# Optimization experiments

Hardware: AMD Instinct MI355X
Metric: run time of the kernel (lower is better)

Reference implementation:

```python
import jax, jax.numpy as jnp
import numpy as np

HEADS = 8
HEAD_DIM = 160
L_TXT = 77
C = 3  # number of erased target concepts
SIG_A, SIG_B, SIG_C = 10.0, 0.5, 1.0
EPS = 1e-8


def setup_inputs() -> dict:
    key = jax.random.key(0)
    ks = jax.random.split(key, 8)
    B, S, D, DX = 8, 1024, 1280, 768
    return {
        "hidden_states": jax.random.normal(ks[0], (B, S, D), jnp.float32),
        "encoder_hidden_states": jax.random.normal(ks[1], (B, L_TXT, DX), jnp.float32),
        "Wq": jax.random.normal(ks[2], (D, D), jnp.float32) * 0.02,
        "Wk": jax.random.normal(ks[3], (DX, D), jnp.float32) * 0.02,
        "Wv": jax.random.normal(ks[4], (DX, D), jnp.float32) * 0.02,
        "Wo": jax.random.normal(ks[5], (D, D), jnp.float32) * 0.02,
        "bo": jnp.zeros((D,), jnp.float32),
        "target_value": jax.random.normal(ks[7], (2 * C * HEADS, L_TXT, HEAD_DIM), jnp.float32),
    }


def _head_to_batch(x):
    B, S, D = x.shape
    return x.reshape(B, S, HEADS, D // HEADS).transpose(0, 2, 1, 3).reshape(B * HEADS, S, D // HEADS)


def _ortho_decomp_retain(v, target_value):
    # v: [M, 77, d]  (M = batch*heads, with batch = 2*R from CFG)
    d = HEAD_DIM
    hd = 16 * d
    # regroup target records: [2*C*8,77,d] -> [C,16,77,d]
    tar = target_value.reshape(2, C, HEADS, L_TXT, d).transpose(1, 0, 2, 3, 4).reshape(C, 16, L_TXT, d)
    T = tar.transpose(2, 0, 1, 3).reshape(L_TXT, C, hd)  # [77, C, 16d] per-token concept vectors
    # one-step Gram-Schmidt projection matrix per token (uses ORIGINAL V_j, as in source)
    G = jnp.einsum('lcd,led->lce', T, T)                  # [77, C, C] Gram matrix
    diag = jnp.einsum('lcc->lc', G)                       # [77, C]
    Pm = jnp.eye(C, dtype=v.dtype) - jnp.tril(G / diag[:, None, :], -1)  # [77, C, C]
    OB = jnp.einsum('lce,led->lcd', Pm, T)                # ortho basis [77, C, 16d]
    # regroup current value into records of 16 (=2*8) maps
    M = v.shape[0]
    R = M // 16
    cur = v.reshape(2, R, HEADS, L_TXT, d).transpose(1, 0, 2, 3, 4).reshape(R, 16, L_TXT, d)
    pro = cur.transpose(0, 2, 1, 3).reshape(R, L_TXT, hd)  # [R, 77, 16d]
    dot1 = jnp.einsum('lcd,rld->rlc', OB, pro)             # [R, 77, C]
    dot2 = jnp.sum(OB * OB, axis=-1)                       # [77, C]
    w = jnp.nan_to_num(dot1 / dot2)
    w = w.at[:, 0, :].set(0.0)                             # weight[0].fill_(0): zero token 0 (BOS)
    # token_sim: cosine similarity + sigmoid gating
    nT = jnp.maximum(jnp.linalg.norm(T, axis=-1), EPS)     # [77, C]
    nP = jnp.maximum(jnp.linalg.norm(pro, axis=-1), EPS)   # [R, 77]
    cos = jnp.einsum('lcd,rld->rlc', T, pro) / (nT[None] * nP[:, :, None])
    cos = SIG_C / (1.0 + jnp.exp(-SIG_A * (cos - SIG_B)))
    PB = jnp.einsum('lce,rled->rlcd', Pm, cos[..., None] * T)  # projected basis [R,77,C,16d]
    era = jnp.einsum('rlc,rlcd->rld', w, PB)               # [R, 77, 16d]
    era = era.reshape(R, L_TXT, 16, d).transpose(0, 2, 1, 3)  # [R, 16, 77, d]
    ret = cur - era                                        # retain branch
    return ret.reshape(R, 2, HEADS, L_TXT, d).transpose(1, 0, 2, 3, 4).reshape(M, L_TXT, d)


def reference(hidden_states, encoder_hidden_states, Wq, Wk, Wv, Wo, bo, target_value):
    B, S, D = hidden_states.shape
    q = _head_to_batch(hidden_states @ Wq)            # [B*h, S, d]
    k = _head_to_batch(encoder_hidden_states @ Wk)    # [B*h, 77, d]
    v = _head_to_batch(encoder_hidden_states @ Wv)    # [B*h, 77, d]
    scale = 1.0 / jnp.sqrt(jnp.asarray(HEAD_DIM, q.dtype))
    probs = jax.nn.softmax(jnp.einsum('bqd,bkd->bqk', q, k) * scale, axis=-1)
    v = _ortho_decomp_retain(v, target_value)         # concept-erased (retain) values
    hs = jnp.einsum('bqk,bkd->bqd', probs, v)         # [B*h, S, d]
    hs = hs.reshape(B, HEADS, S, HEAD_DIM).transpose(0, 2, 1, 3).reshape(B, S, D)
    return hs @ Wo + bo
```

## Files before the change

### kernel.cpp

```cpp
#include <hip/hip_runtime.h>
#include <hip/hip_bf16.h>
#include <math.h>

#define BATCH   8
#define S_LEN   1024
#define D_MODEL 1280
#define DX      768
#define NH      8
#define HD      160
#define LTXT    77
#define NBH     (BATCH*NH)
#define MKV_PAD 640
#define MQ      (BATCH*S_LEN)
#define MKV     (BATCH*LTXT)

typedef _Float16 f16x8 __attribute__((ext_vector_type(8)));
typedef _Float16 f16x4 __attribute__((ext_vector_type(4)));
typedef float    f32x4 __attribute__((ext_vector_type(4)));

#define NB_HID 10240
#define NB_ENC 480
#define NB_WQ  1600
#define NB_WO  1600
#define NB_WK  960
#define NB_WV  960
#define NB_PREP (NB_HID+NB_ENC+NB_WQ+NB_WO+NB_WK+NB_WV)

__device__ inline void to_f16_dev(const float* __restrict__ X,
                                  _Float16* __restrict__ Y,
                                  int K, int Mreal, int bid)
{
    const size_t g = ((size_t)bid * 256 + threadIdx.x) * 4;
    const int row = (int)(g / K);
    float4 x = make_float4(0.f, 0.f, 0.f, 0.f);
    if (row < Mreal) x = *(const float4*)&X[g];
    f16x4 o;
    o[0] = (_Float16)x.x; o[1] = (_Float16)x.y;
    o[2] = (_Float16)x.z; o[3] = (_Float16)x.w;
    *(f16x4*)&Y[g] = o;
}

__device__ inline void wt_t_dev(const float* __restrict__ W,
                                _Float16* __restrict__ BT,
                                int K, int N, int KLD, int noff,
                                int bx, int by, float (*tile)[33])
{
    const int k0 = by * 32, n0 = bx * 32;
    const int tx = threadIdx.x & 31, ty = threadIdx.x >> 5;
#pragma unroll
    for (int r = 0; r < 32; r += 8)
        tile[r + ty][tx] = W[(size_t)(k0 + r + ty) * N + n0 + tx];
    __syncthreads();
#pragma unroll
    for (int r = 0; r < 32; r += 8) {
        const int n = noff + n0 + r + ty, k = k0 + tx;
        BT[(size_t)n * KLD + k] = (_Float16)tile[tx][r + ty];
    }
}

__global__ __launch_bounds__(256) void prep_kernel(
    const float* __restrict__ hidden, const float* __restrict__ enc,
    const float* __restrict__ Wq, const float* __restrict__ Wk,
    const float* __restrict__ Wv, const float* __restrict__ Wo,
    _Float16* __restrict__ hidf, _Float16* __restrict__ encb,
    _Float16* __restrict__ B2Tq, _Float16* __restrict__ B2To,
    _Float16* __restrict__ B2Tkv)
{
    __shared__ float tile[32][33];
    int bid = blockIdx.x;
    if (bid < NB_HID) { to_f16_dev(hidden, hidf, D_MODEL, MQ, bid); return; }
    bid -= NB_HID;
    if (bid < NB_ENC) { to_f16_dev(enc, encb, DX, MKV, bid); return; }
    bid -= NB_ENC;
    if (bid < NB_WQ)  { wt_t_dev(Wq, B2Tq, D_MODEL, D_MODEL, D_MODEL, 0, bid % 40, bid / 40, tile); return; }
    bid -= NB_WQ;
    if (bid < NB_WO)  { wt_t_dev(Wo, B2To, D_MODEL, D_MODEL, D_MODEL, 0, bid % 40, bid / 40, tile); return; }
    bid -= NB_WO;
    if (bid < NB_WK)  { wt_t_dev(Wk, B2Tkv, DX, D_MODEL, DX, 0, bid % 40, bid / 40, tile); return; }
    bid -= NB_WK;
    wt_t_dev(Wv, B2Tkv, DX, D_MODEL, DX, D_MODEL, bid % 40, bid / 40, tile);
}

__device__ inline void async_copy16(const void* gptr, void* lptr) {
    __builtin_amdgcn_global_load_lds(
        (const __attribute__((address_space(1))) unsigned*)gptr,
        (__attribute__((address_space(3))) unsigned*)lptr, 16, 0, 0);
}

__global__ __launch_bounds__(256) void gemm_mfma_bt(
    const _Float16* __restrict__ A, const _Float16* __restrict__ B,
    float* __restrict__ Cf, _Float16* __restrict__ Cb,
    _Float16* __restrict__ kout, float* __restrict__ vout,
    int Mreal, int N, int KK, int ntn, const float* __restrict__ bias)
{
    __shared__ __align__(16) _Float16 As[128 * 64];
    __shared__ __align__(16) _Float16 Bs[128 * 64];
    const int t = threadIdx.x;
    const int wave = t >> 6, lane = t & 63;
    const int lr = lane & 15, lg = lane >> 4;
    const int wr = wave >> 1, wc = wave & 1;

    const int nwg = gridDim.x;
    const int q = nwg >> 3, r = nwg & 7;
    const int xcd = blockIdx.x & 7, idx = blockIdx.x >> 3;
    const int swz = (xcd < r ? xcd * (q + 1) : r * (q + 1) + (xcd - r) * q) + idx;
    const int m0 = (swz / ntn) * 128, n0 = (swz % ntn) * 128;

    f32x4 acc[4][4] = {};

    const int sr = lane >> 3;
    const int sk = 8 * ((lane & 7) ^ sr);

    for (int k0 = 0; k0 < KK; k0 += 64) {
        __syncthreads();
#pragma unroll
        for (int s = 0; s < 4; ++s) {
            const int ti = wave * 4 + s;
            const int row = ti * 8 + sr;
            async_copy16(A + (size_t)(m0 + row) * KK + k0 + sk, As + ti * 512);
            async_copy16(B + (size_t)(n0 + row) * KK + k0 + sk, Bs + ti * 512);
        }
        __syncthreads();

        f16x8 af[4][2], bf_[4][2];
#pragma unroll
        for (int i = 0; i < 4; ++i)
#pragma unroll
            for (int ki = 0; ki < 2; ++ki) {
                const int koff = (ki * 32 + lg * 8) ^ ((lr & 7) * 8);
                af[i][ki]  = *(const f16x8*)(As + (wr * 64 + i * 16 + lr) * 64 + koff);
                bf_[i][ki] = *(const f16x8*)(Bs + (wc * 64 + i * 16 + lr) * 64 + koff);
            }
#pragma unroll
        for (int ki = 0; ki < 2; ++ki)
#pragma unroll
            for (int i = 0; i < 4; ++i)
#pragma unroll
                for (int j = 0; j < 4; ++j)
                    acc[i][j] = __builtin_amdgcn_mfma_f32_16x16x32_f16(
                        af[i][ki], bf_[j][ki], acc[i][j], 0, 0, 0);
    }

#pragma unroll
    for (int i = 0; i < 4; ++i) {
#pragma unroll
        for (int j = 0; j < 4; ++j) {
            const int col = n0 + wc * 64 + j * 16 + lr;
            const float bv = bias ? bias[col] : 0.f;
#pragma unroll
            for (int rr = 0; rr < 4; ++rr) {
                const int row = m0 + wr * 64 + i * 16 + lg * 4 + rr;
                const float v = acc[i][j][rr] + bv;
                if (kout) {
                    if (row < Mreal) {
                        if (col < D_MODEL) kout[(size_t)row * D_MODEL + col] = (_Float16)v;
                        else               vout[(size_t)row * D_MODEL + col - D_MODEL] = v;
                    }
                } else if (Cb) {
                    Cb[(size_t)row * N + col] = (_Float16)v;
                } else {
                    Cf[(size_t)row * N + col] = v;
                }
            }
        }
    }
}

#define GQ_BLOCKS  ((MQ/128)*(D_MODEL/128))
#define GKV_BLOCKS ((MKV_PAD/128)*(2*D_MODEL/128))

__global__ __launch_bounds__(256) void retain_kernel(
    const float* __restrict__ vbuf, _Float16* __restrict__ vf16,
    const float* __restrict__ tv)
{
    const int l = blockIdx.x % LTXT;
    const int r = blockIdx.x / LTXT;
    const int t = threadIdx.x;

    float g00=0,g01=0,g02=0,g11=0,g12=0,g22=0,tp0=0,tp1=0,tp2=0,pp=0;
    float p_save[10], t0s[10], t1s[10], t2s[10];
#pragma unroll
    for (int it = 0; it < 10; ++it) {
        const int j   = t + it * 256;
        const int m16 = j / HD, d = j % HD;
        const int e = m16 >> 3, h = m16 & 7;
        const float T0 = tv[((size_t)(e*24 +  0 + h) * LTXT + l) * HD + d];
        const float T1 = tv[((size_t)(e*24 +  8 + h) * LTXT + l) * HD + d];
        const float T2 = tv[((size_t)(e*24 + 16 + h) * LTXT + l) * HD + d];
        const float p  = vbuf[((size_t)((e*4 + r) * LTXT + l)) * D_MODEL + h*HD + d];
        p_save[it] = p; t0s[it] = T0; t1s[it] = T1; t2s[it] = T2;
        g00 += T0*T0; g01 += T0*T1; g02 += T0*T2;
        g11 += T1*T1; g12 += T1*T2; g22 += T2*T2;
        tp0 += T0*p;  tp1 += T1*p;  tp2 += T2*p;  pp += p*p;
    }

    __shared__ float part[4][10];
    const int wave = t >> 6, lane = t & 63;
    float vals[10] = {g00,g01,g02,g11,g12,g22,tp0,tp1,tp2,pp};
#pragma unroll
    for (int i = 0; i < 10; ++i) {
        float x = vals[i];
        x += __shfl_down(x, 32); x += __shfl_down(x, 16);
        x += __shfl_down(x,  8); x += __shfl_down(x,  4);
        x += __shfl_down(x,  2); x += __shfl_down(x,  1);
        if (lane == 0) part[wave][i] = x;
    }
    __syncthreads();

    float s[10];
#pragma unroll
    for (int i = 0; i < 10; ++i)
        s[i] = part[0][i] + part[1][i] + part[2][i] + part[3][i];

    const float G[3][3] = {{s[0],s[1],s[2]},{s[1],s[3],s[4]},{s[2],s[4],s[5]}};
    const float tp[3] = {s[6], s[7], s[8]};
    const float ppv = s[9];

    float Pm[3][3];
#pragma unroll
    for (int c = 0; c < 3; ++c)
#pragma unroll
        for (int e = 0; e < 3; ++e) {
            float v = (c == e) ? 1.f : 0.f;
            if (c > e) v -= G[c][e] / G[e][e];
            Pm[c][e] = v;
        }

    const float nP = fmaxf(sqrtf(ppv), 1e-8f);
    float w[3], cosg[3];
#pragma unroll
    for (int c = 0; c < 3; ++c) {
        const float nT = fmaxf(sqrtf(G[c][c]), 1e-8f);
        const float cosv = tp[c] / (nT * nP);
        cosg[c] = 1.f / (1.f + expf(-10.f * (cosv - 0.5f)));
        float d1 = Pm[c][0]*tp[0] + Pm[c][1]*tp[1] + Pm[c][2]*tp[2];
        float d2 = 0.f;
#pragma unroll
        for (int e = 0; e < 3; ++e)
#pragma unroll
            for (int f = 0; f < 3; ++f) d2 += Pm[c][e] * Pm[c][f] * G[e][f];
        float wc = d1 / d2;
        if (isnan(wc)) wc = 0.f;
        if (l == 0)    wc = 0.f;
        w[c] = wc;
    }

    float coef[3];
#pragma unroll
    for (int e = 0; e < 3; ++e)
        coef[e] = cosg[e] * (w[0]*Pm[0][e] + w[1]*Pm[1][e] + w[2]*Pm[2][e]);

#pragma unroll
    for (int it = 0; it < 10; ++it) {
        const int j   = t + it * 256;
        const int m16 = j / HD, d = j % HD;
        const int e = m16 >> 3, h = m16 & 7;
        const float era = coef[0]*t0s[it] + coef[1]*t1s[it] + coef[2]*t2s[it];
        vf16[((size_t)((e*4 + r) * LTXT + l)) * D_MODEL + h*HD + d] =
            (_Float16)(p_save[it] - era);
    }
}

#define KSTRIDE 168
#define VSTRIDE 104
#define PSTRIDE 104

__global__ __launch_bounds__(256, 3) void attn_mfma(
    const _Float16* __restrict__ qb,
    const _Float16* __restrict__ kf,
    const _Float16* __restrict__ vf,
    _Float16* __restrict__ hs)
{
    __shared__ _Float16 KV[160 * VSTRIDE];
    __shared__ _Float16 Ps[4][16 * PSTRIDE];
    const int bh = blockIdx.x, b = bh >> 3, h = bh & 7;
    const int qt = blockIdx.y;
    const int t = threadIdx.x, wave = t >> 6, lane = t & 63;
    const int lr = lane & 15, lg = lane >> 4;

    for (int c = t; c < 1600; c += 256) {
        const int l = c / 20, d8 = (c % 20) * 8;
        f16x8 u;
#pragma unroll
        for (int i = 0; i < 8; ++i) u[i] = (_Float16)0.f;
        if (l < LTXT) u = *(const f16x8*)&kf[((size_t)(b * LTXT + l)) * D_MODEL + h * HD + d8];
        *(f16x8*)&KV[l * KSTRIDE + d8] = u;
    }
    {
        for (int i = lane; i < 256; i += 64)
            Ps[wave][(i >> 4) * PSTRIDE + 80 + (i & 15)] = (_Float16)0.f;
    }
    __syncthreads();

    const int qrow0 = b * S_LEN + qt * 64 + wave * 16;
    const _Float16* qp = qb + (size_t)(qrow0 + lr) * D_MODEL + h * HD;
    f16x8 af[5];
#pragma unroll
    for (int kt = 0; kt < 5; ++kt)
        af[kt] = *(const f16x8*)&qp[kt * 32 + lg * 8];

    f32x4 accs[5] = {};
#pragma unroll
    for (int j = 0; j < 5; ++j)
#pragma unroll
        for (int kt = 0; kt < 5; ++kt) {
            const f16x8 bf = *(const f16x8*)&KV[(j * 16 + lr) * KSTRIDE + kt * 32 + lg * 8];
            accs[j] = __builtin_amdgcn_mfma_f32_16x16x32_f16(af[kt], bf, accs[j], 0, 0, 0);
        }

    float s[5][4];
    const float scale = 0.07905694150420949f;
#pragma unroll
    for (int j = 0; j < 5; ++j)
#pragma unroll
        for (int r = 0; r < 4; ++r)
            s[j][r] = accs[j][r] * scale;
    if (lr >= 13) { s[4][0] = -1e30f; s[4][1] = -1e30f; s[4][2] = -1e30f; s[4][3] = -1e30f; }

    float rsum[4];
#pragma unroll
    for (int r = 0; r < 4; ++r) {
        float m = s[0][r];
#pragma unroll
        for (int j = 1; j < 5; ++j) m = fmaxf(m, s[j][r]);
        m = fmaxf(m, __shfl_xor(m, 1));
        m = fmaxf(m, __shfl_xor(m, 2));
        m = fmaxf(m, __shfl_xor(m, 4));
        m = fmaxf(m, __shfl_xor(m, 8));
        float sum = 0.f;
#pragma unroll
        for (int j = 0; j < 5; ++j) {
            const float p = __expf(s[j][r] - m);
            s[j][r] = p;
            sum += p;
        }
        sum += __shfl_xor(sum, 1);
        sum += __shfl_xor(sum, 2);
        sum += __shfl_xor(sum, 4);
        sum += __shfl_xor(sum, 8);
        rsum[r] = sum;
    }

#pragma unroll
    for (int j = 0; j < 5; ++j)
#pragma unroll
        for (int r = 0; r < 4; ++r)
            Ps[wave][(lg * 4 + r) * PSTRIDE + j * 16 + lr] = (_Float16)s[j][r];

    __syncthreads();

    for (int c = t; c < 1920; c += 256) {
        const int l = c / 20, d8 = (c % 20) * 8;
        f16x8 vv;
#pragma unroll
        for (int i = 0; i < 8; ++i) vv[i] = (_Float16)0.f;
        if (l < LTXT) vv = *(const f16x8*)&vf[((size_t)(b * LTXT + l)) * D_MODEL + h * HD + d8];
#pragma unroll
        for (int i = 0; i < 8; ++i)
            KV[(d8 + i) * VSTRIDE + l] = vv[i];
    }
    __syncthreads();

    f16x8 pa[3];
#pragma unroll
    for (int kt = 0; kt < 3; ++kt)
        pa[kt] = *(const f16x8*)&Ps[wave][lr * PSTRIDE + kt * 32 + lg * 8];
    f32x4 acch[10] = {};
#pragma unroll
    for (int dt = 0; dt < 10; ++dt)
#pragma unroll
        for (int kt = 0; kt < 3; ++kt) {
            const f16x8 vb = *(const f16x8*)&KV[(dt * 16 + lr) * VSTRIDE + kt * 32 + lg * 8];
            acch[dt] = __builtin_amdgcn_mfma_f32_16x16x32_f16(pa[kt], vb, acch[dt], 0, 0, 0);
        }

    const float inv[4] = {1.f / rsum[0], 1.f / rsum[1], 1.f / rsum[2], 1.f / rsum[3]};
#pragma unroll
    for (int dt = 0; dt < 10; ++dt) {
        const int col = h * HD + dt * 16 + lr;
#pragma unroll
        for (int r = 0; r < 4; ++r) {
            const int row = qrow0 + lg * 4 + r;
            hs[(size_t)row * D_MODEL + col] = (_Float16)(acch[dt][r] * inv[r]);
        }
    }
}

extern "C" void kernel_launch(void* const* d_in, const int* in_sizes, int n_in,
                              void* d_out, int out_size, void* d_ws, size_t ws_size,
                              hipStream_t stream)
{
    const float* hidden = (const float*)d_in[0];
    const float* enc    = (const float*)d_in[1];
    const float* Wq     = (const float*)d_in[2];
    const float* Wk     = (const float*)d_in[3];
    const float* Wv     = (const float*)d_in[4];
    const float* Wo     = (const float*)d_in[5];
    const float* bo     = (const float*)d_in[6];
    const float* tv     = (const float*)d_in[7];
    float* out = (float*)d_out;

    _Float16* kf     = (_Float16*)d_ws;
    float*    vbuf   = (float*)(kf + (size_t)MKV * D_MODEL);
    _Float16* vf16   = (_Float16*)(vbuf + (size_t)MKV * D_MODEL);
    _Float16* qf     = vf16 + (size_t)MKV * D_MODEL;
    _Float16* hsf    = qf   + (size_t)MQ * D_MODEL;
    _Float16* hidf   = hsf  + (size_t)MQ * D_MODEL;
    _Float16* encb   = hidf + (size_t)MQ * D_MODEL;
    _Float16* B2Tq   = encb + (size_t)MKV_PAD * DX;
    _Float16* B2To   = B2Tq + (size_t)D_MODEL * D_MODEL;
    _Float16* B2Tkv  = B2To + (size_t)D_MODEL * D_MODEL;

    prep_kernel<<<NB_PREP, 256, 0, stream>>>(
        hidden, enc, Wq, Wk, Wv, Wo, hidf, encb, B2Tq, B2To, B2Tkv);

    gemm_mfma_bt<<<GQ_BLOCKS, 256, 0, stream>>>(
        hidf, B2Tq, nullptr, qf, nullptr, nullptr,
        MQ, D_MODEL, D_MODEL, D_MODEL / 128, nullptr);

    gemm_mfma_bt<<<GKV_BLOCKS, 256, 0, stream>>>(
        encb, B2Tkv, nullptr, nullptr, kf, vbuf,
        MKV, 2 * D_MODEL, DX, 2 * D_MODEL / 128, nullptr);

    retain_kernel<<<4 * LTXT, 256, 0, stream>>>(vbuf, vf16, tv);

    attn_mfma<<<dim3(NBH, S_LEN / 64), 256, 0, stream>>>(qf, kf, vf16, hsf);

    gemm_mfma_bt<<<GQ_BLOCKS, 256, 0, stream>>>(
        hsf, B2To, out, nullptr, nullptr, nullptr,
        MQ, D_MODEL, D_MODEL, D_MODEL / 128, bo);
}
```

Before: 160.7 us.

## Fold Wq into K and Wo into V to skip full Q and output projections

```diff
diff --git a/kernel.cpp b/kernel.cpp
--- a/kernel.cpp
+++ b/kernel.cpp
@@ -9,10 +9,13 @@
 #define NH      8
 #define HD      160
 #define LTXT    77
-#define NBH     (BATCH*NH)
 #define MKV_PAD 640
 #define MQ      (BATCH*S_LEN)
 #define MKV     (BATCH*LTXT)
+#define HL      80
+#define NHL     640
+#define KPAD    192
+#define KVROWS  5184
 
 typedef _Float16 f16x8 __attribute__((ext_vector_type(8)));
 typedef _Float16 f16x4 __attribute__((ext_vector_type(4)));
@@ -20,11 +23,13 @@
 
 #define NB_HID 10240
 #define NB_ENC 480
-#define NB_WQ  1600
-#define NB_WO  1600
+#define NB_WQP 1600
+#define NB_WOT 1600
 #define NB_WK  960
 #define NB_WV  960
-#define NB_PREP (NB_HID+NB_ENC+NB_WQ+NB_WO+NB_WK+NB_WV)
+#define NB_ZK  972
+#define NB_ZV  972
+#define NB_PREP (NB_HID+NB_ENC+NB_WQP+NB_WOT+NB_WK+NB_WV+NB_ZK+NB_ZV)
 
 __device__ inline void to_f16_dev(const float* __restrict__ X,
                                   _Float16* __restrict__ Y,
@@ -40,6 +45,15 @@
     *(f16x4*)&Y[g] = o;
 }
 
+__device__ inline void zero_f16_dev(_Float16* __restrict__ Y, int bid)
+{
+    const size_t g = ((size_t)bid * 256 + threadIdx.x) * 4;
+    f16x4 z;
+    z[0] = (_Float16)0.f; z[1] = (_Float16)0.f;
+    z[2] = (_Float16)0.f; z[3] = (_Float16)0.f;
+    *(f16x4*)&Y[g] = z;
+}
+
 __device__ inline void wt_t_dev(const float* __restrict__ W,
                                 _Float16* __restrict__ BT,
                                 int K, int N, int KLD, int noff,
@@ -63,8 +77,9 @@
     const float* __restrict__ Wq, const float* __restrict__ Wk,
     const float* __restrict__ Wv, const float* __restrict__ Wo,
     _Float16* __restrict__ hidf, _Float16* __restrict__ encb,
-    _Float16* __restrict__ B2Tq, _Float16* __restrict__ B2To,
-    _Float16* __restrict__ B2Tkv)
+    _Float16* __restrict__ Wqp, _Float16* __restrict__ WoT,
+    _Float16* __restrict__ B2Tkv,
+    _Float16* __restrict__ kf2, _Float16* __restrict__ vf2)
 {
     __shared__ float tile[32][33];
     int bid = blockIdx.x;
@@ -72,13 +87,17 @@
     bid -= NB_HID;
     if (bid < NB_ENC) { to_f16_dev(enc, encb, DX, MKV, bid); return; }
     bid -= NB_ENC;
-    if (bid < NB_WQ)  { wt_t_dev(Wq, B2Tq, D_MODEL, D_MODEL, D_MODEL, 0, bid % 40, bid / 40, tile); return; }
-    bid -= NB_WQ;
-    if (bid < NB_WO)  { wt_t_dev(Wo, B2To, D_MODEL, D_MODEL, D_MODEL, 0, bid % 40, bid / 40, tile); return; }
-    bid -= NB_WO;
+    if (bid < NB_WQP) { to_f16_dev(Wq, Wqp, D_MODEL, D_MODEL, bid); return; }
+    bid -= NB_WQP;
+    if (bid < NB_WOT) { wt_t_dev(Wo, WoT, D_MODEL, D_MODEL, D_MODEL, 0, bid % 40, bid / 40, tile); return; }
+    bid -= NB_WOT;
     if (bid < NB_WK)  { wt_t_dev(Wk, B2Tkv, DX, D_MODEL, DX, 0, bid % 40, bid / 40, tile); return; }
     bid -= NB_WK;
-    wt_t_dev(Wv, B2Tkv, DX, D_MODEL, DX, D_MODEL, bid % 40, bid / 40, tile);
+    if (bid < NB_WV)  { wt_t_dev(Wv, B2Tkv, DX, D_MODEL, DX, D_MODEL, bid % 40, bid / 40, tile); return; }
+    bid -= NB_WV;
+    if (bid < NB_ZK)  { zero_f16_dev(kf2, bid); return; }
+    bid -= NB_ZK;
+    zero_f16_dev(vf2, bid);
 }
 
 __device__ inline void async_copy16(const void* gptr, void* lptr) {
@@ -89,9 +108,9 @@
 
 __global__ __launch_bounds__(256) void gemm_mfma_bt(
     const _Float16* __restrict__ A, const _Float16* __restrict__ B,
-    float* __restrict__ Cf, _Float16* __restrict__ Cb,
-    _Float16* __restrict__ kout, float* __restrict__ vout,
-    int Mreal, int N, int KK, int ntn, const float* __restrict__ bias)
+    float* __restrict__ Cf, _Float16* __restrict__ kout, float* __restrict__ vout,
+    const float* __restrict__ bias,
+    int Mreal, int N, int KK, int ntn, int tpb, int AB, int BB, int CB)
 {
     __shared__ __align__(16) _Float16 As[128 * 64];
     __shared__ __align__(16) _Float16 Bs[128 * 64];
@@ -104,7 +123,11 @@
     const int q = nwg >> 3, r = nwg & 7;
     const int xcd = blockIdx.x & 7, idx = blockIdx.x >> 3;
     const int swz = (xcd < r ? xcd * (q + 1) : r * (q + 1) + (xcd - r) * q) + idx;
-    const int m0 = (swz / ntn) * 128, n0 = (swz % ntn) * 128;
+    const int b  = swz / tpb;
+    const int lc = swz % tpb;
+    const int m0 = (lc / ntn) * 128, n0 = (lc % ntn) * 128;
+    const size_t arow0 = (size_t)b * AB + m0;
+    const size_t brow0 = (size_t)b * BB + n0;
 
     f32x4 acc[4][4] = {};
 
@@ -117,8 +140,8 @@
         for (int s = 0; s < 4; ++s) {
             const int ti = wave * 4 + s;
             const int row = ti * 8 + sr;
-            async_copy16(A + (size_t)(m0 + row) * KK + k0 + sk, As + ti * 512);
-            async_copy16(B + (size_t)(n0 + row) * KK + k0 + sk, Bs + ti * 512);
+            async_copy16(A + (arow0 + row) * KK + k0 + sk, As + ti * 512);
+            async_copy16(B + (brow0 + row) * KK + k0 + sk, Bs + ti * 512);
         }
         __syncthreads();
 
@@ -153,24 +176,104 @@
                 const float v = acc[i][j][rr] + bv;
                 if (kout) {
                     if (row < Mreal) {
-                        if (col < D_MODEL) kout[(size_t)row * D_MODEL + col] = (_Float16)v;
-                        else               vout[(size_t)row * D_MODEL + col - D_MODEL] = v;
+                        if (col < D_MODEL) {
+                            const int h = col / HD, d = col % HD;
+                            const int bb = row / LTXT, ll = row % LTXT;
+                            kout[((size_t)((bb * 8 + h) * LTXT + ll)) * KPAD + d] = (_Float16)v;
+                        } else {
+                            vout[(size_t)row * D_MODEL + col - D_MODEL] = v;
+                        }
                     }
-                } else if (Cb) {
-                    Cb[(size_t)row * N + col] = (_Float16)v;
                 } else {
-                    Cf[(size_t)row * N + col] = v;
+                    Cf[((size_t)(b * CB + row)) * N + col] = v;
                 }
             }
         }
     }
 }
 
-#define GQ_BLOCKS  ((MQ/128)*(D_MODEL/128))
-#define GKV_BLOCKS ((MKV_PAD/128)*(2*D_MODEL/128))
+__global__ __launch_bounds__(256) void gemm_small(
+    const _Float16* __restrict__ A, const _Float16* __restrict__ B,
+    _Float16* __restrict__ Co,
+    int mtn, int ntn, int Mg, int Ng,
+    int astride, int bstride, int ostride,
+    int aBH, int bBH, int aH, int bH,
+    int oB, int oH, int oC)
+{
+    __shared__ __align__(16) _Float16 As[128 * 64];
+    __shared__ __align__(16) _Float16 Bs[128 * 64];
+    const int t = threadIdx.x;
+    const int wave = t >> 6, lane = t & 63;
+    const int lr = lane & 15, lg = lane >> 4;
+    const int wr = wave >> 1, wc = wave & 1;
+
+    const int nwg = gridDim.x;
+    const int q = nwg >> 3, r = nwg & 7;
+    const int xcd = blockIdx.x & 7, idx = blockIdx.x >> 3;
+    const int swz = (xcd < r ? xcd * (q + 1) : r * (q + 1) + (xcd - r) * q) + idx;
+    const int tpb = mtn * ntn;
+    const int bh = swz / tpb;
+    const int lc = swz % tpb;
+    const int m0 = (lc / ntn) * 128, n0 = (lc % ntn) * 128;
+    const int b = bh >> 3, h = bh & 7;
+
+    const size_t abase = (size_t)bh * aBH + m0;
+    const size_t bbase = (size_t)bh * bBH + n0;
+    const int aoff = h * aH, boff = h * bH;
+
+    f32x4 acc[4][4] = {};
+
+    const int sr = lane >> 3;
+    const int sk = 8 * ((lane & 7) ^ sr);
+
+    for (int k0 = 0; k0 < KPAD; k0 += 64) {
+        __syncthreads();
+#pragma unroll
+        for (int s = 0; s < 4; ++s) {
+            const int ti = wave * 4 + s;
+            const int row = ti * 8 + sr;
+            async_copy16(A + (abase + row) * astride + aoff + k0 + sk, As + ti * 512);
+            async_copy16(B + (bbase + row) * bstride + boff + k0 + sk, Bs + ti * 512);
+        }
+        __syncthreads();
+
+        f16x8 af[4][2], bf_[4][2];
+#pragma unroll
+        for (int i = 0; i < 4; ++i)
+#pragma unroll
+            for (int ki = 0; ki < 2; ++ki) {
+                const int koff = (ki * 32 + lg * 8) ^ ((lr & 7) * 8);
+                af[i][ki]  = *(const f16x8*)(As + (wr * 64 + i * 16 + lr) * 64 + koff);
+                bf_[i][ki] = *(const f16x8*)(Bs + (wc * 64 + i * 16 + lr) * 64 + koff);
+            }
+#pragma unroll
+        for (int ki = 0; ki < 2; ++ki)
+#pragma unroll
+            for (int i = 0; i < 4; ++i)
+#pragma unroll
+                for (int j = 0; j < 4; ++j)
+                    acc[i][j] = __builtin_amdgcn_mfma_f32_16x16x32_f16(
+                        af[i][ki], bf_[j][ki], acc[i][j], 0, 0, 0);
+    }
+
+#pragma unroll
+    for (int i = 0; i < 4; ++i) {
+#pragma unroll
+        for (int j = 0; j < 4; ++j) {
+            const int n = n0 + wc * 64 + j * 16 + lr;
+#pragma unroll
+            for (int rr = 0; rr < 4; ++rr) {
+                const int m = m0 + wr * 64 + i * 16 + lg * 4 + rr;
+                if (m < Mg && n < Ng)
+                    Co[((size_t)(b * oB + h * oH + m)) * ostride + h * oC + n] =
+                        (_Float16)acc[i][j][rr];
+            }
+        }
+    }
+}
 
 __global__ __launch_bounds__(256) void retain_kernel(
-    const float* __restrict__ vbuf, _Float16* __restrict__ vf16,
+    const float* __restrict__ vbuf, _Float16* __restrict__ vf2,
     const float* __restrict__ tv)
 {
     const int l = blockIdx.x % LTXT;
@@ -256,133 +359,51 @@
         const int m16 = j / HD, d = j % HD;
         const int e = m16 >> 3, h = m16 & 7;
         const float era = coef[0]*t0s[it] + coef[1]*t1s[it] + coef[2]*t2s[it];
-        vf16[((size_t)((e*4 + r) * LTXT + l)) * D_MODEL + h*HD + d] =
+        vf2[((size_t)(((e*4 + r) * 8 + h) * LTXT + l)) * KPAD + d] =
             (_Float16)(p_save[it] - era);
     }
 }
 
-#define KSTRIDE 168
-#define VSTRIDE 104
-#define PSTRIDE 104
-
-__global__ __launch_bounds__(256, 3) void attn_mfma(
-    const _Float16* __restrict__ qb,
-    const _Float16* __restrict__ kf,
-    const _Float16* __restrict__ vf,
-    _Float16* __restrict__ hs)
-{
-    __shared__ _Float16 KV[160 * VSTRIDE];
-    __shared__ _Float16 Ps[4][16 * PSTRIDE];
-    const int bh = blockIdx.x, b = bh >> 3, h = bh & 7;
-    const int qt = blockIdx.y;
-    const int t = threadIdx.x, wave = t >> 6, lane = t & 63;
-    const int lr = lane & 15, lg = lane >> 4;
-
-    for (int c = t; c < 1600; c += 256) {
-        const int l = c / 20, d8 = (c % 20) * 8;
-        f16x8 u;
-#pragma unroll
-        for (int i = 0; i < 8; ++i) u[i] = (_Float16)0.f;
-        if (l < LTXT) u = *(const f16x8*)&kf[((size_t)(b * LTXT + l)) * D_MODEL + h * HD + d8];
-        *(f16x8*)&KV[l * KSTRIDE + d8] = u;
-    }
-    {
-        for (int i = lane; i < 256; i += 64)
-            Ps[wave][(i >> 4) * PSTRIDE + 80 + (i & 15)] = (_Float16)0.f;
-    }
-    __syncthreads();
-
-    const int qrow0 = b * S_LEN + qt * 64 + wave * 16;
-    const _Float16* qp = qb + (size_t)(qrow0 + lr) * D_MODEL + h * HD;
-    f16x8 af[5];
-#pragma unroll
-    for (int kt = 0; kt < 5; ++kt)
-        af[kt] = *(const f16x8*)&qp[kt * 32 + lg * 8];
-
-    f32x4 accs[5] = {};
-#pragma unroll
-    for (int j = 0; j < 5; ++j)
-#pragma unroll
-        for (int kt = 0; kt < 5; ++kt) {
-            const f16x8 bf = *(const f16x8*)&KV[(j * 16 + lr) * KSTRIDE + kt * 32 + lg * 8];
-            accs[j] = __builtin_amdgcn_mfma_f32_16x16x32_f16(af[kt], bf, accs[j], 0, 0, 0);
-        }
-
-    float s[5][4];
+__global__ __launch_bounds__(256) void softmax_kernel(
+    const float* __restrict__ sc, _Float16* __restrict__ P)
+{
+    const int row = blockIdx.x * 4 + (threadIdx.x >> 6);
+    const int lane = threadIdx.x & 63;
+    const int s = lane & 7;
+    const float* rp = sc + (size_t)row * NHL + lane * 10;
+    float v[10];
+#pragma unroll
+    for (int j = 0; j < 10; ++j) v[j] = rp[j];
+    const int nreal = (s == 7) ? 7 : 10;
+
+    float mx = -1e30f;
+#pragma unroll
+    for (int j = 0; j < 10; ++j) if (j < nreal) mx = fmaxf(mx, v[j]);
+    mx = fmaxf(mx, __shfl_xor(mx, 1));
+    mx = fmaxf(mx, __shfl_xor(mx, 2));
+    mx = fmaxf(mx, __shfl_xor(mx, 4));
+
     const float scale = 0.07905694150420949f;
-#pragma unroll
-    for (int j = 0; j < 5; ++j)
-#pragma unroll
-        for (int r = 0; r < 4; ++r)
-            s[j][r] = accs[j][r] * scale;
-    if (lr >= 13) { s[4][0] = -1e30f; s[4][1] = -1e30f; s[4][2] = -1e30f; s[4][3] = -1e30f; }
-
-    float rsum[4];
-#pragma unroll
-    for (int r = 0; r < 4; ++r) {
-        float m = s[0][r];
-#pragma unroll
-        for (int j = 1; j < 5; ++j) m = fmaxf(m, s[j][r]);
-        m = fmaxf(m, __shfl_xor(m, 1));
-        m = fmaxf(m, __shfl_xor(m, 2));
-        m = fmaxf(m, __shfl_xor(m, 4));
-        m = fmaxf(m, __shfl_xor(m, 8));
-        float sum = 0.f;
-#pragma unroll
-        for (int j = 0; j < 5; ++j) {
-            const float p = __expf(s[j][r] - m);
-            s[j][r] = p;
-            sum += p;
-        }
-        sum += __shfl_xor(sum, 1);
-        sum += __shfl_xor(sum, 2);
-        sum += __shfl_xor(sum, 4);
-        sum += __shfl_xor(sum, 8);
-        rsum[r] = sum;
-    }
-
-#pragma unroll
-    for (int j = 0; j < 5; ++j)
-#pragma unroll
-        for (int r = 0; r < 4; ++r)
-            Ps[wave][(lg * 4 + r) * PSTRIDE + j * 16 + lr] = (_Float16)s[j][r];
-
-    __syncthreads();
-
-    for (int c = t; c < 1920; c += 256) {
-        const int l = c / 20, d8 = (c % 20) * 8;
-        f16x8 vv;
-#pragma unroll
-        for (int i = 0; i < 8; ++i) vv[i] = (_Float16)0.f;
-        if (l < LTXT) vv = *(const f16x8*)&vf[((size_t)(b * LTXT + l)) * D_MODEL + h * HD + d8];
-#pragma unroll
-        for (int i = 0; i < 8; ++i)
-            KV[(d8 + i) * VSTRIDE + l] = vv[i];
-    }
-    __syncthreads();
-
-    f16x8 pa[3];
-#pragma unroll
-    for (int kt = 0; kt < 3; ++kt)
-        pa[kt] = *(const f16x8*)&Ps[wave][lr * PSTRIDE + kt * 32 + lg * 8];
-    f32x4 acch[10] = {};
-#pragma unroll
-    for (int dt = 0; dt < 10; ++dt)
-#pragma unroll
-        for (int kt = 0; kt < 3; ++kt) {
-            const f16x8 vb = *(const f16x8*)&KV[(dt * 16 + lr) * VSTRIDE + kt * 32 + lg * 8];
-            acch[dt] = __builtin_amdgcn_mfma_f32_16x16x32_f16(pa[kt], vb, acch[dt], 0, 0, 0);
-        }
-
-    const float inv[4] = {1.f / rsum[0], 1.f / rsum[1], 1.f / rsum[2], 1.f / rsum[3]};
-#pragma unroll
-    for (int dt = 0; dt < 10; ++dt) {
-        const int col = h * HD + dt * 16 + lr;
-#pragma unroll
-        for (int r = 0; r < 4; ++r) {
-            const int row = qrow0 + lg * 4 + r;
-            hs[(size_t)row * D_MODEL + col] = (_Float16)(acch[dt][r] * inv[r]);
-        }
+    float sum = 0.f;
+#pragma unroll
+    for (int j = 0; j < 10; ++j) {
+        const float e = (j < nreal) ? __expf((v[j] - mx) * scale) : 0.f;
+        v[j] = e; sum += e;
+    }
+    sum += __shfl_xor(sum, 1);
+    sum += __shfl_xor(sum, 2);
+    sum += __shfl_xor(sum, 4);
+    const float inv = 1.f / sum;
+
+    _Float16* op = P + (size_t)row * NHL + lane * 10;
+#pragma unroll
+    for (int j = 0; j < 5; ++j) {
+        const _Float16 a = (_Float16)(v[2*j] * inv);
+        const _Float16 b = (_Float16)(v[2*j+1] * inv);
+        ushort2 u;
+        u.x = *(const unsigned short*)&a;
+        u.y = *(const unsigned short*)&b;
+        *(ushort2*)(op + 2*j) = u;
     }
 }
 
@@ -400,33 +421,49 @@
     const float* tv     = (const float*)d_in[7];
     float* out = (float*)d_out;
 
-    _Float16* kf     = (_Float16*)d_ws;
-    float*    vbuf   = (float*)(kf + (size_t)MKV * D_MODEL);
-    _Float16* vf16   = (_Float16*)(vbuf + (size_t)MKV * D_MODEL);
-    _Float16* qf     = vf16 + (size_t)MKV * D_MODEL;
-    _Float16* hsf    = qf   + (size_t)MQ * D_MODEL;
-    _Float16* hidf   = hsf  + (size_t)MQ * D_MODEL;
-    _Float16* encb   = hidf + (size_t)MQ * D_MODEL;
-    _Float16* B2Tq   = encb + (size_t)MKV_PAD * DX;
-    _Float16* B2To   = B2Tq + (size_t)D_MODEL * D_MODEL;
-    _Float16* B2Tkv  = B2To + (size_t)D_MODEL * D_MODEL;
+    _Float16* kf2   = (_Float16*)d_ws;
+    _Float16* vf2   = kf2 + (size_t)KVROWS * KPAD;
+    float*    vbuf  = (float*)(vf2 + (size_t)KVROWS * KPAD);
+    _Float16* Wqp   = (_Float16*)(vbuf + (size_t)MKV * D_MODEL);
+    _Float16* WoT   = Wqp + (size_t)D_MODEL * D_MODEL + 192;
+    _Float16* B2Tkv = WoT + (size_t)D_MODEL * D_MODEL + 192;
+    _Float16* encb  = B2Tkv + (size_t)2 * D_MODEL * DX;
+    _Float16* Sb    = encb + (size_t)MKV_PAD * DX;
+    _Float16* Vt    = Sb + (size_t)BATCH * NHL * D_MODEL;
+    float*    scores= (float*)(Vt + (size_t)BATCH * D_MODEL * NHL);
+    _Float16* hidf  = (_Float16*)(scores + (size_t)MQ * NHL);
+    _Float16* Pt    = hidf;
 
     prep_kernel<<<NB_PREP, 256, 0, stream>>>(
-        hidden, enc, Wq, Wk, Wv, Wo, hidf, encb, B2Tq, B2To, B2Tkv);
-
-    gemm_mfma_bt<<<GQ_BLOCKS, 256, 0, stream>>>(
-        hidf, B2Tq, nullptr, qf, nullptr, nullptr,
-        MQ, D_MODEL, D_MODEL, D_MODEL / 128, nullptr);
-
-    gemm_mfma_bt<<<GKV_BLOCKS, 256, 0, stream>>>(
-        encb, B2Tkv, nullptr, nullptr, kf, vbuf,
-        MKV, 2 * D_MODEL, DX, 2 * D_MODEL / 128, nullptr);
-
-    retain_kernel<<<4 * LTXT, 256, 0, stream>>>(vbuf, vf16, tv);
-
-    attn_mfma<<<dim3(NBH, S_LEN / 64), 256, 0, stream>>>(qf, kf, vf16, hsf);
-
-    gemm_mfma_bt<<<GQ_BLOCKS, 256, 0, stream>>>(
-        hsf, B2To, out, nullptr, nullptr, nullptr,
-        MQ, D_MODEL, D_MODEL, D_MODEL / 128, bo);
-}
+        hidden, enc, Wq, Wk, Wv, Wo, hidf, encb, Wqp, WoT, B2Tkv, kf2, vf2);
+
+    gemm_mfma_bt<<<100, 256, 0, stream>>>(
+        encb, B2Tkv, nullptr, kf2, vbuf, nullptr,
+        MKV, 2 * D_MODEL, DX, 20, 100, 0, 0, 0);
+
+    retain_kernel<<<4 * LTXT, 256, 0, stream>>>(vbuf, vf2, tv);
+
+    gemm_small<<<640, 256, 0, stream>>>(
+        kf2, Wqp, Sb,
+         1, 10,  LTXT, D_MODEL,
+         KPAD, D_MODEL, D_MODEL,
+         LTXT, 0,  0, HD,
+         NHL, HL, 0);
+
+    gemm_small<<<640, 256, 0, stream>>>(
+        WoT, vf2, Vt,
+         10, 1,  D_MODEL, LTXT,
+         D_MODEL, KPAD, NHL,
+         0, LTXT,  HD, 0,
+         D_MODEL, 0, HL);
+
+    gemm_mfma_bt<<<320, 256, 0, stream>>>(
+        hidf, Sb, scores, nullptr, nullptr, nullptr,
+        1024, NHL, D_MODEL, 5, 40, 1024, NHL, 1024);
+
+    softmax_kernel<<<MQ / 4, 256, 0, stream>>>(scores, Pt);
+
+    gemm_mfma_bt<<<640, 256, 0, stream>>>(
+        Pt, Vt, out, nullptr, nullptr, bo,
+        1024, D_MODEL, NHL, 10, 80, 1024, D_MODEL, 1024);
+}
```

Measured after the change: 138.7 us. 13.7% less time.
